# Optimization experiments

Hardware: AMD Instinct MI355X
Metric: run time of the kernel (lower is better)

The kernel has to match this reference:

```python
import jax, jax.numpy as jnp
import numpy as np

N = 50000        # nodes
E = 1_600_000    # edges (avg degree 32)
G = 512          # graphs
F_IN = 9         # node features
H = 64           # hidden dim
ED = 1           # edge feature dim


def _lin(k, fo, fi):
    w = jax.random.normal(k, (fo, fi), jnp.float32) * (1.0 / np.sqrt(fi))
    b = jnp.zeros((fo,), jnp.float32)
    return w, b


def setup_inputs() -> dict:
    key = jax.random.key(0)
    ks = jax.random.split(key, 16)
    x = jax.random.normal(ks[0], (N, F_IN), jnp.float32)
    edge_index = jax.random.randint(ks[1], (2, E), 0, N, dtype=jnp.int64)
    edge_attr = jax.random.normal(ks[2], (E, ED), jnp.float32)
    batch = jnp.sort(jax.random.randint(ks[3], (N,), 0, G, dtype=jnp.int64))
    B_total = jax.random.uniform(ks[4], (G,), jnp.float32) * 100.0
    terminal_mask = jax.random.randint(ks[5], (N,), 0, 2, dtype=jnp.int32)
    c_cost = jax.random.uniform(ks[6], (N,), jnp.float32)
    # conv1: edge lin (ED->F_IN), nn = Linear(F_IN,H), Linear(H,H)
    e1_w, e1_b = _lin(ks[7], F_IN, ED)
    w1a, b1a = _lin(ks[8], H, F_IN)
    w1b, b1b = _lin(ks[9], H, H)
    # conv2: edge lin (ED->H), nn = Linear(H,H), Linear(H,H)
    e2_w, e2_b = _lin(ks[10], H, ED)
    w2a, b2a = _lin(ks[11], H, H)
    w2b, b2b = _lin(ks[12], H, H)
    # readout: Linear(H,H//2), Linear(H//2,1)
    wr1, br1 = _lin(ks[13], H // 2, H)
    wr2, br2 = _lin(ks[14], 1, H // 2)
    return dict(x=x, edge_index=edge_index, edge_attr=edge_attr, batch=batch,
                B_total=B_total, terminal_mask=terminal_mask, c_cost=c_cost,
                e1_w=e1_w, e1_b=e1_b, w1a=w1a, b1a=b1a, w1b=w1b, b1b=b1b,
                e2_w=e2_w, e2_b=e2_b, w2a=w2a, b2a=b2a, w2b=w2b, b2b=b2b,
                wr1=wr1, br1=br1, wr2=wr2, br2=br2)


def _gine(x, src, dst, edge_attr, ew, eb, wa, ba, wb, bb):
    # GINEConv (eps=0): nn(x + sum_j relu(x_j + W_e e_ji))
    e = edge_attr @ ew.T + eb                    # [E, F]
    m = jax.nn.relu(x[src] + e)                  # [E, F] gather + edge fuse
    aggr = jax.ops.segment_sum(m, dst, num_segments=N)  # scatter-add -> [N, F]
    h = x + aggr
    h = jax.nn.relu(h @ wa.T + ba)
    h = jax.nn.relu(h @ wb.T + bb)
    return h


def reference(x, edge_index, edge_attr, batch, B_total, terminal_mask, c_cost,
              e1_w, e1_b, w1a, b1a, w1b, b1b,
              e2_w, e2_b, w2a, b2a, w2b, b2b,
              wr1, br1, wr2, br2):
    src, dst = edge_index[0], edge_index[1]
    h = _gine(x, src, dst, edge_attr, e1_w, e1_b, w1a, b1a, w1b, b1b)
    h = _gine(h, src, dst, edge_attr, e2_w, e2_b, w2a, b2a, w2b, b2b)
    pi_raw = jax.nn.sigmoid((jax.nn.relu(h @ wr1.T + br1) @ wr2.T + br2))[:, 0]
    pi_raw = pi_raw * (1.0 - terminal_mask.astype(jnp.float32))
    node_expenses = pi_raw * c_cost
    total_expenses = jax.ops.segment_sum(node_expenses, batch, num_segments=G)
    ratio = jnp.minimum(B_total[batch] / (total_expenses[batch] + 1e-12), 1.0)
    return pi_raw * ratio
```

## Files before the change

kernel.cpp:

```cpp
#include <hip/hip_runtime.h>
#include <hip/hip_fp16.h>
#include <math.h>

#define N_NODES 50000
#define N_EDGES 1600000
#define N_GRAPHS 512
#define F_IN 9
#define H 64
#define N_BUCKETS ((N_NODES + 255) >> 8)
#define EPB 4096
#define N_SBLK ((N_EDGES + EPB - 1) / EPB)
#define FINE_CAP 10240

typedef _Float16 f16x8 __attribute__((ext_vector_type(8)));
typedef float f32x4 __attribute__((ext_vector_type(4)));

__device__ __forceinline__ void pack_weights_body(
        const float* __restrict__ w1a, const float* __restrict__ w1b,
        const float* __restrict__ w2a, const float* __restrict__ w2b,
        const float* __restrict__ wr1,
        __half* __restrict__ pk1Ah, __half* __restrict__ pk1Al,
        __half* __restrict__ pk1Bh, __half* __restrict__ pk1Bl,
        __half* __restrict__ pkAh, __half* __restrict__ pkAl,
        __half* __restrict__ pkBh, __half* __restrict__ pkBl,
        __half* __restrict__ pkRh, __half* __restrict__ pkRl) {
    int t = threadIdx.x;
    for (int i = t; i < 2048; i += 512) {
        int j = i & 7, l = (i >> 3) & 63, tt = i >> 9;
        int q = l >> 4, n = l & 15;
        int k = q * 8 + j;
        float v = (k < F_IN) ? w1a[(tt * 16 + n) * F_IN + k] : 0.f;
        __half h = __float2half(v);
        pk1Ah[i] = h; pk1Al[i] = __float2half(v - __half2float(h));
    }
    for (int i = t; i < 4096; i += 512) {
        int j = i & 7, l = (i >> 3) & 63, c = (i >> 9) & 1, tt = i >> 10;
        int q = l >> 4, n = l & 15;
        int src = (tt * 16 + n) * H + c * 32 + q * 8 + j;
        float v1 = w1b[src], wa = w2a[src], wb = w2b[src];
        __half h1 = __float2half(v1), ah = __float2half(wa), bh = __float2half(wb);
        pk1Bh[i] = h1; pk1Bl[i] = __float2half(v1 - __half2float(h1));
        pkAh[i] = ah; pkAl[i] = __float2half(wa - __half2float(ah));
        pkBh[i] = bh; pkBl[i] = __float2half(wb - __half2float(bh));
    }
    for (int i = t; i < 2048; i += 512) {
        int j = i & 7, l = (i >> 3) & 63, c = (i >> 9) & 1, tt = i >> 10;
        int q = l >> 4, n = l & 15;
        float wr = wr1[(tt * 16 + n) * H + c * 32 + q * 8 + j];
        __half rh = __float2half(wr);
        pkRh[i] = rh; pkRl[i] = __float2half(wr - __half2float(rh));
    }
}

__global__ void __launch_bounds__(512)
bucket_scatter(const int* __restrict__ ei,
               const float* __restrict__ ea,
               int* __restrict__ bnext,
               uint2* __restrict__ ebuk,
               const float* __restrict__ w1a,
               const float* __restrict__ w1b,
               const float* __restrict__ w2a,
               const float* __restrict__ w2b,
               const float* __restrict__ wr1,
               __half* pk1Ah, __half* pk1Al,
               __half* pk1Bh, __half* pk1Bl,
               __half* pkAh, __half* pkAl,
               __half* pkBh, __half* pkBl,
               __half* pkRh, __half* pkRl) {
    if (blockIdx.x == 0) {
        pack_weights_body(w1a, w1b, w2a, w2b, wr1, pk1Ah, pk1Al, pk1Bh, pk1Bl,
                          pkAh, pkAl, pkBh, pkBl, pkRh, pkRl);
        return;
    }
    __shared__ int cnt[N_BUCKETS];
    __shared__ int gbase[N_BUCKETS];
    for (int i = threadIdx.x; i < N_BUCKETS; i += 512) cnt[i] = 0;
    __syncthreads();
    int base = (blockIdx.x - 1) * EPB;
    int rk[8];
    unsigned pay[8];
#pragma unroll
    for (int j = 0; j < 8; ++j) {
        int e = base + j * 512 + threadIdx.x;
        rk[j] = -1;
        if (e < N_EDGES) {
            int d = ei[N_EDGES + e];
            int s = ei[e];
            float a = ea[e];
            pay[j] = ((unsigned)s << 16) |
                     (unsigned)__half_as_ushort(__float2half(a));
            int b = d >> 8;
            int r = atomicAdd(&cnt[b], 1);
            rk[j] = (b << 21) | ((d & 255) << 13) | r;
        }
    }
    __syncthreads();
    for (int i = threadIdx.x; i < N_BUCKETS; i += 512)
        gbase[i] = cnt[i] ? atomicAdd(&bnext[i], cnt[i]) : 0;
    __syncthreads();
#pragma unroll
    for (int j = 0; j < 8; ++j) {
        if (rk[j] < 0) continue;
        int b = rk[j] >> 21, dl = (rk[j] >> 13) & 255, r = rk[j] & 8191;
        int slot = gbase[b] + r;
        if (slot >= FINE_CAP) continue;
        ebuk[(size_t)b * FINE_CAP + slot] = make_uint2(pay[j], (unsigned)dl);
    }
}

__global__ void __launch_bounds__(512)
bucket_fine(const uint2* __restrict__ ebuk,
            const int* __restrict__ bnext,
            unsigned* __restrict__ ep4,
            int* __restrict__ starts, int* __restrict__ deg) {
    __shared__ unsigned sorted[FINE_CAP];
    __shared__ int cntN[256], offN[256], nxtN[256];
    __shared__ int wsum[4];
    int b = blockIdx.x;
    int base = b * FINE_CAP;
    int count = bnext[b];
    if (count > FINE_CAP) count = FINE_CAP;
    int tid = threadIdx.x;
    if (tid < 256) cntN[tid] = 0;
    __syncthreads();
    uint2 ev[20];
#pragma unroll
    for (int k = 0; k < 20; ++k) {
        int i = tid + k * 512;
        ev[k] = (i < count) ? ebuk[base + i] : make_uint2(0u, 0xFFFFFFFFu);
    }
#pragma unroll
    for (int k = 0; k < 20; ++k)
        if (ev[k].y < 256u) atomicAdd(&cntN[ev[k].y], 1);
    __syncthreads();
    int lane = tid & 63, wid = tid >> 6;
    int v = 0, incl = 0;
    if (tid < 256) {
        v = cntN[tid]; incl = v;
#pragma unroll
        for (int off = 1; off < 64; off <<= 1) {
            int t = __shfl_up(incl, off, 64);
            if (lane >= off) incl += t;
        }
        if (lane == 63) wsum[wid] = incl;
    }
    __syncthreads();
    if (tid < 256) {
        int woff = 0;
        for (int w = 0; w < wid; ++w) woff += wsum[w];
        int excl = woff + incl - v;
        offN[tid] = excl;
        nxtN[tid] = 0;
        int n = (b << 8) + tid;
        if (n < N_NODES) { starts[n] = base + excl; deg[n] = v; }
    }
    __syncthreads();
#pragma unroll
    for (int k = 0; k < 20; ++k) {
        if (ev[k].y < 256u) {
            int r = atomicAdd(&nxtN[ev[k].y], 1);
            sorted[offN[ev[k].y] + r] = ev[k].x;
        }
    }
    __syncthreads();
    for (int i = tid; i < count; i += 512)
        ep4[base + i] = sorted[i];
}

#define UNPACK_ATTR(P) __half2float(__ushort_as_half((unsigned short)((P) & 0xffffu)))

__global__ void agg1_kernel(const float* __restrict__ x,
                            const int* __restrict__ starts,
                            const int* __restrict__ deg,
                            const unsigned* __restrict__ ep4,
                            const float* __restrict__ e1w,
                            const float* __restrict__ e1b,
                            float* __restrict__ xs) {
    int n = blockIdx.x * (blockDim.x >> 6) + (threadIdx.x >> 6);
    int lane = threadIdx.x & 63;
    if (n >= N_NODES) return;
    int slot = lane >> 4;
    int f = lane & 15;
    int s0 = starts[n], dg = deg[n];
    bool act = f < F_IN;
    float wf = act ? e1w[f] : 0.f;
    float bf = act ? e1b[f] : 0.f;
    float acc = 0.f;
    int j = slot;
    for (; j + 12 < dg; j += 16) {
        unsigned pa = ep4[s0 + j];
        unsigned pb = ep4[s0 + j + 4];
        unsigned pc = ep4[s0 + j + 8];
        unsigned pd = ep4[s0 + j + 12];
        float xa_ = act ? x[(pa >> 16) * F_IN + f] : 0.f;
        float xb_ = act ? x[(pb >> 16) * F_IN + f] : 0.f;
        float xc_ = act ? x[(pc >> 16) * F_IN + f] : 0.f;
        float xd_ = act ? x[(pd >> 16) * F_IN + f] : 0.f;
        if (act) {
            acc += fmaxf(xa_ + UNPACK_ATTR(pa) * wf + bf, 0.f)
                 + fmaxf(xb_ + UNPACK_ATTR(pb) * wf + bf, 0.f)
                 + fmaxf(xc_ + UNPACK_ATTR(pc) * wf + bf, 0.f)
                 + fmaxf(xd_ + UNPACK_ATTR(pd) * wf + bf, 0.f);
        }
    }
    for (; j < dg; j += 4) {
        unsigned p = ep4[s0 + j];
        float xv = act ? x[(p >> 16) * F_IN + f] : 0.f;
        float m = xv + UNPACK_ATTR(p) * wf + bf;
        acc += act ? fmaxf(m, 0.f) : 0.f;
    }
    acc += __shfl_xor(acc, 16, 64);
    acc += __shfl_xor(acc, 32, 64);
    if (lane < 32)
        xs[n * 32 + lane] = (lane < F_IN) ? x[n * F_IN + lane] + acc : 0.f;
}

__device__ __forceinline__ void split8(const float* __restrict__ v,
                                       f16x8& hi, f16x8& lo) {
#pragma unroll
    for (int j = 0; j < 8; ++j) {
        _Float16 h = (_Float16)v[j];
        hi[j] = h;
        lo[j] = (_Float16)(v[j] - (float)h);
    }
}

#define TILE3(C, A0H, A0L, A1H, A1L, PH, PL, T) do {                          \
        f16x8 b0h = *(const f16x8*)((PH) + (((T) * 2 + 0) * 64 + lane) * 8);  \
        f16x8 b0l = *(const f16x8*)((PL) + (((T) * 2 + 0) * 64 + lane) * 8);  \
        f16x8 b1h = *(const f16x8*)((PH) + (((T) * 2 + 1) * 64 + lane) * 8);  \
        f16x8 b1l = *(const f16x8*)((PL) + (((T) * 2 + 1) * 64 + lane) * 8);  \
        C = __builtin_amdgcn_mfma_f32_16x16x32_f16(A0H, b0h, C, 0, 0, 0);     \
        C = __builtin_amdgcn_mfma_f32_16x16x32_f16(A0L, b0h, C, 0, 0, 0);     \
        C = __builtin_amdgcn_mfma_f32_16x16x32_f16(A0H, b0l, C, 0, 0, 0);     \
        C = __builtin_amdgcn_mfma_f32_16x16x32_f16(A1H, b1h, C, 0, 0, 0);     \
        C = __builtin_amdgcn_mfma_f32_16x16x32_f16(A1L, b1h, C, 0, 0, 0);     \
        C = __builtin_amdgcn_mfma_f32_16x16x32_f16(A1H, b1l, C, 0, 0, 0);     \
    } while (0)

__global__ void node1_kernel(const float* __restrict__ xs,
                             const __half* __restrict__ pk1Ah, const __half* __restrict__ pk1Al,
                             const float* __restrict__ b1a,
                             const __half* __restrict__ pk1Bh, const __half* __restrict__ pk1Bl,
                             const float* __restrict__ b1b,
                             __half* __restrict__ h1) {
    __shared__ float hbuf[4][16][68];
    int wv = threadIdx.x >> 6;
    int lane = threadIdx.x & 63;
    int gwave = blockIdx.x * 4 + wv;
    bool active = gwave < (N_NODES / 16);
    int base = active ? gwave * 16 : 0;
    int m = lane & 15, q = lane >> 4;
    const _Float16* pAh = (const _Float16*)pk1Ah;
    const _Float16* pAl = (const _Float16*)pk1Al;
    const _Float16* pBh = (const _Float16*)pk1Bh;
    const _Float16* pBl = (const _Float16*)pk1Bl;

    f16x8 ah, al;
    split8(xs + (size_t)(base + m) * 32 + q * 8, ah, al);
#pragma unroll
    for (int t = 0; t < 4; ++t) {
        f32x4 c = {0.f, 0.f, 0.f, 0.f};
        f16x8 bh = *(const f16x8*)(pAh + (t * 64 + lane) * 8);
        f16x8 bl = *(const f16x8*)(pAl + (t * 64 + lane) * 8);
        c = __builtin_amdgcn_mfma_f32_16x16x32_f16(ah, bh, c, 0, 0, 0);
        c = __builtin_amdgcn_mfma_f32_16x16x32_f16(al, bh, c, 0, 0, 0);
        c = __builtin_amdgcn_mfma_f32_16x16x32_f16(ah, bl, c, 0, 0, 0);
        float bias = b1a[t * 16 + m];
#pragma unroll
        for (int r = 0; r < 4; ++r)
            hbuf[wv][q * 4 + r][t * 16 + m] = fmaxf(c[r] + bias, 0.f);
    }
    __syncthreads();
    f16x8 a0h, a0l, a1h, a1l;
    split8(&hbuf[wv][m][q * 8], a0h, a0l);
    split8(&hbuf[wv][m][32 + q * 8], a1h, a1l);
    float tmp[4][4];
#pragma unroll
    for (int t = 0; t < 4; ++t) {
        f32x4 c = {0.f, 0.f, 0.f, 0.f};
        TILE3(c, a0h, a0l, a1h, a1l, pBh, pBl, t);
        float bias = b1b[t * 16 + m];
#pragma unroll
        for (int r = 0; r < 4; ++r)
            tmp[t][r] = fmaxf(c[r] + bias, 0.f);
    }
    __syncthreads();
#pragma unroll
    for (int t = 0; t < 4; ++t)
#pragma unroll
        for (int r = 0; r < 4; ++r)
            hbuf[wv][q * 4 + r][t * 16 + m] = tmp[t][r];
    __syncthreads();
    if (active) {
        int nn = lane >> 2, part = lane & 3;
        f16x8 vlo, vhi;
        const float* rlo = &hbuf[wv][nn][part * 8];
        const float* rhi = &hbuf[wv][nn][32 + part * 8];
#pragma unroll
        for (int j = 0; j < 8; ++j) {
            vlo[j] = (_Float16)rlo[j];
            vhi[j] = (_Float16)rhi[j];
        }
        *(f16x8*)(h1 + (size_t)(base + nn) * 64 + part * 8) = vlo;
        *(f16x8*)(h1 + (size_t)(base + nn) * 64 + 32 + part * 8) = vhi;
    }
}

__global__ void aggphase2_kernel(const __half* __restrict__ h1,
                                 const int* __restrict__ starts,
                                 const int* __restrict__ deg,
                                 const unsigned* __restrict__ ep4,
                                 const float* __restrict__ ew,
                                 const float* __restrict__ eb,
                                 float* __restrict__ htot) {
    int xcd = blockIdx.x & 7;
    int hoff = (xcd >> 2) * 32;
    int grp = (blockIdx.x >> 3) * 4 + (xcd & 3);
    int wv = threadIdx.x >> 6;
    int n = grp * 4 + wv;
    int lane = threadIdx.x & 63;
    if (n >= N_NODES) return;
    int par = lane >> 5;
    int fh = lane & 31;
    int f = hoff + fh;
    int s0 = starts[n], dg = deg[n];
    const unsigned* ep = ep4 + s0;
    float wf = ew[f], bf = eb[f];
    float acc = 0.f;
#define EDGE1(P, V) acc += fmaxf((V) + UNPACK_ATTR(P) * wf + bf, 0.f)
    int j = 0;
    for (; j + 16 <= dg; j += 16) {
        unsigned p0 = ep[j +  0 + par], p1 = ep[j +  2 + par];
        unsigned p2 = ep[j +  4 + par], p3 = ep[j +  6 + par];
        unsigned p4 = ep[j +  8 + par], p5 = ep[j + 10 + par];
        unsigned p6 = ep[j + 12 + par], p7 = ep[j + 14 + par];
        float v0 = __half2float(h1[(size_t)(p0 >> 16) * 64 + f]);
        float v1 = __half2float(h1[(size_t)(p1 >> 16) * 64 + f]);
        float v2 = __half2float(h1[(size_t)(p2 >> 16) * 64 + f]);
        float v3 = __half2float(h1[(size_t)(p3 >> 16) * 64 + f]);
        float v4 = __half2float(h1[(size_t)(p4 >> 16) * 64 + f]);
        float v5 = __half2float(h1[(size_t)(p5 >> 16) * 64 + f]);
        float v6 = __half2float(h1[(size_t)(p6 >> 16) * 64 + f]);
        float v7 = __half2float(h1[(size_t)(p7 >> 16) * 64 + f]);
        EDGE1(p0, v0); EDGE1(p1, v1); EDGE1(p2, v2); EDGE1(p3, v3);
        EDGE1(p4, v4); EDGE1(p5, v5); EDGE1(p6, v6); EDGE1(p7, v7);
    }
    for (; j + 2 <= dg; j += 2) {
        unsigned p = ep[j + par];
        float v = __half2float(h1[(size_t)(p >> 16) * 64 + f]);
        EDGE1(p, v);
    }
    if (j < dg && par == 0) {
        unsigned p = ep[j];
        float v = __half2float(h1[(size_t)(p >> 16) * 64 + f]);
        EDGE1(p, v);
    }
#undef EDGE1
    acc += __shfl_xor(acc, 32, 64);
    if (par == 0) {
        float self = __half2float(h1[(size_t)n * 64 + f]);
        htot[(size_t)n * 64 + f] = self + acc;
    }
}

__global__ void node2_kernel(const float* __restrict__ htot,
                             const __half* __restrict__ pkAh, const __half* __restrict__ pkAl,
                             const float* __restrict__ b2a,
                             const __half* __restrict__ pkBh, const __half* __restrict__ pkBl,
                             const float* __restrict__ b2b,
                             const __half* __restrict__ pkRh, const __half* __restrict__ pkRl,
                             const float* __restrict__ br1,
                             const float* __restrict__ wr2,
                             const float* __restrict__ br2,
                             const int* __restrict__ term,
                             const int* __restrict__ batch,
                             const float* __restrict__ ccost,
                             float* __restrict__ pi,
                             float* __restrict__ te) {
    __shared__ float hbuf[4][16][68];
    int wv = threadIdx.x >> 6;
    int lane = threadIdx.x & 63;
    int gwave = blockIdx.x * 4 + wv;
    bool active = gwave < (N_NODES / 16);
    int base = active ? gwave * 16 : 0;
    int m = lane & 15, q = lane >> 4;
    const _Float16* pAh = (const _Float16*)pkAh;
    const _Float16* pAl = (const _Float16*)pkAl;
    const _Float16* pBh = (const _Float16*)pkBh;
    const _Float16* pBl = (const _Float16*)pkBl;
    const _Float16* pRh = (const _Float16*)pkRh;
    const _Float16* pRl = (const _Float16*)pkRl;

    f16x8 a0h, a0l, a1h, a1l;
    {
        const float* hrow = htot + (size_t)(base + m) * 64;
        split8(hrow + q * 8, a0h, a0l);
        split8(hrow + 32 + q * 8, a1h, a1l);
    }
#pragma unroll
    for (int t = 0; t < 4; ++t) {
        f32x4 c = {0.f, 0.f, 0.f, 0.f};
        TILE3(c, a0h, a0l, a1h, a1l, pAh, pAl, t);
        float bias = b2a[t * 16 + m];
#pragma unroll
        for (int r = 0; r < 4; ++r)
            hbuf[wv][q * 4 + r][t * 16 + m] = fmaxf(c[r] + bias, 0.f);
    }
    __syncthreads();
    split8(&hbuf[wv][m][q * 8], a0h, a0l);
    split8(&hbuf[wv][m][32 + q * 8], a1h, a1l);
    float tmp[4][4];
#pragma unroll
    for (int t = 0; t < 4; ++t) {
        f32x4 c = {0.f, 0.f, 0.f, 0.f};
        TILE3(c, a0h, a0l, a1h, a1l, pBh, pBl, t);
        float bias = b2b[t * 16 + m];
#pragma unroll
        for (int r = 0; r < 4; ++r)
            tmp[t][r] = fmaxf(c[r] + bias, 0.f);
    }
    __syncthreads();
#pragma unroll
    for (int t = 0; t < 4; ++t)
#pragma unroll
        for (int r = 0; r < 4; ++r)
            hbuf[wv][q * 4 + r][t * 16 + m] = tmp[t][r];
    __syncthreads();
    split8(&hbuf[wv][m][q * 8], a0h, a0l);
    split8(&hbuf[wv][m][32 + q * 8], a1h, a1l);
    float partial[4] = {0.f, 0.f, 0.f, 0.f};
#pragma unroll
    for (int t = 0; t < 2; ++t) {
        f32x4 c = {0.f, 0.f, 0.f, 0.f};
        TILE3(c, a0h, a0l, a1h, a1l, pRh, pRl, t);
        float bias = br1[t * 16 + m];
        float wv2 = wr2[t * 16 + m];
#pragma unroll
        for (int r = 0; r < 4; ++r)
            partial[r] += fmaxf(c[r] + bias, 0.f) * wv2;
    }
#pragma unroll
    for (int off = 1; off < 16; off <<= 1) {
        partial[0] += __shfl_xor(partial[0], off, 64);
        partial[1] += __shfl_xor(partial[1], off, 64);
        partial[2] += __shfl_xor(partial[2], off, 64);
        partial[3] += __shfl_xor(partial[3], off, 64);
    }
    if (active && m == 0) {
#pragma unroll
        for (int r = 0; r < 4; ++r) {
            int n = base + q * 4 + r;
            float z = partial[r] + br2[0];
            float sig = 1.f / (1.f + expf(-z));
            float pv = sig * (1.f - (float)term[n]);
            pi[n] = pv;
            float contrib = pv * ccost[n];
            if (contrib != 0.f) atomicAdd(&te[batch[n]], contrib);
        }
    }
}

__global__ void final_kernel(const float* __restrict__ pi,
                             const int* __restrict__ batch,
                             const float* __restrict__ Btot,
                             const float* __restrict__ te,
                             float* __restrict__ out) {
    int n = blockIdx.x * blockDim.x + threadIdx.x;
    if (n >= N_NODES) return;
    int b = batch[n];
    float ratio = fminf(Btot[b] / (te[b] + 1e-12f), 1.f);
    out[n] = pi[n] * ratio;
}

extern "C" void kernel_launch(void* const* d_in, const int* in_sizes, int n_in,
                              void* d_out, int out_size, void* d_ws, size_t ws_size,
                              hipStream_t stream) {
    const float* x     = (const float*)d_in[0];
    const int*   ei    = (const int*)d_in[1];
    const float* ea    = (const float*)d_in[2];
    const int*   batch = (const int*)d_in[3];
    const float* Btot  = (const float*)d_in[4];
    const int*   term  = (const int*)d_in[5];
    const float* ccost = (const float*)d_in[6];
    const float* e1w   = (const float*)d_in[7];
    const float* e1b   = (const float*)d_in[8];
    const float* w1a   = (const float*)d_in[9];
    const float* b1a   = (const float*)d_in[10];
    const float* w1b   = (const float*)d_in[11];
    const float* b1b   = (const float*)d_in[12];
    const float* e2w   = (const float*)d_in[13];
    const float* e2b   = (const float*)d_in[14];
    const float* w2a   = (const float*)d_in[15];
    const float* b2a   = (const float*)d_in[16];
    const float* w2b   = (const float*)d_in[17];
    const float* b2b   = (const float*)d_in[18];
    const float* wr1   = (const float*)d_in[19];
    const float* br1   = (const float*)d_in[20];
    const float* wr2   = (const float*)d_in[21];
    const float* br2   = (const float*)d_in[22];

    char* p = (char*)d_ws;
    int*      bnext  = (int*)p;      p += sizeof(int)      * 256;
    float*    te     = (float*)p;    p += sizeof(float)    * N_GRAPHS;
    int*      starts = (int*)p;      p += sizeof(int)      * N_NODES;
    int*      deg    = (int*)p;      p += sizeof(int)      * N_NODES;
    p = (char*)(((size_t)p + 15) & ~(size_t)15);
    uint2*    ebuk   = (uint2*)p;    p += sizeof(uint2)    * (size_t)N_BUCKETS * FINE_CAP;
    unsigned* ep4    = (unsigned*)p; p += sizeof(unsigned) * (size_t)N_BUCKETS * FINE_CAP;
    __half*   h1     = (__half*)p;   p += sizeof(__half)   * (size_t)N_NODES * 64;
    float*    htot   = (float*)p;    p += sizeof(float)    * (size_t)N_NODES * 64;
    float*    xs     = (float*)p;    p += sizeof(float)    * (size_t)N_NODES * 32;
    float*    pi     = (float*)p;    p += sizeof(float)    * N_NODES;
    __half*   pk1Ah  = (__half*)p;   p += sizeof(__half)   * 2048;
    __half*   pk1Al  = (__half*)p;   p += sizeof(__half)   * 2048;
    __half*   pk1Bh  = (__half*)p;   p += sizeof(__half)   * 4096;
    __half*   pk1Bl  = (__half*)p;   p += sizeof(__half)   * 4096;
    __half*   pkAh   = (__half*)p;   p += sizeof(__half)   * 4096;
    __half*   pkAl   = (__half*)p;   p += sizeof(__half)   * 4096;
    __half*   pkBh   = (__half*)p;   p += sizeof(__half)   * 4096;
    __half*   pkBl   = (__half*)p;   p += sizeof(__half)   * 4096;
    __half*   pkRh   = (__half*)p;   p += sizeof(__half)   * 2048;
    __half*   pkRl   = (__half*)p;   p += sizeof(__half)   * 2048;
    float*    out    = (float*)d_out;

    hipMemsetAsync(d_ws, 0, sizeof(int) * 256 + sizeof(float) * N_GRAPHS, stream);

    bucket_scatter<<<1 + N_SBLK, 512, 0, stream>>>(ei, ea, bnext, ebuk,
                                                   w1a, w1b, w2a, w2b, wr1,
                                                   pk1Ah, pk1Al, pk1Bh, pk1Bl,
                                                   pkAh, pkAl, pkBh, pkBl, pkRh, pkRl);
    bucket_fine<<<N_BUCKETS, 512, 0, stream>>>(ebuk, bnext, ep4, starts, deg);
    agg1_kernel<<<(N_NODES + 3) / 4, 256, 0, stream>>>(x, starts, deg, ep4, e1w, e1b, xs);
    node1_kernel<<<(N_NODES / 16 + 3) / 4, 256, 0, stream>>>(xs, pk1Ah, pk1Al, b1a,
                                                             pk1Bh, pk1Bl, b1b, h1);
    aggphase2_kernel<<<25000, 256, 0, stream>>>(h1, starts, deg, ep4,
                                                e2w, e2b, htot);
    node2_kernel<<<(N_NODES / 16 + 3) / 4, 256, 0, stream>>>(htot,
                                                             pkAh, pkAl, b2a,
                                                             pkBh, pkBl, b2b,
                                                             pkRh, pkRl, br1,
                                                             wr2, br2, term,
                                                             batch, ccost, pi, te);
    final_kernel<<<(N_NODES + 255) / 256, 256, 0, stream>>>(pi, batch, Btot, te, out);
}
```

Measured before the change: 265.3 us.

## Process full 64-feature rows per wave in layer-2 aggregation with half2 gathers

The layer-2 aggregation kernel no longer splits each node's 64 features across two XCD-mapped blocks. Each wave now handles a whole node, with each lane reading a half2 (two features) per gathered neighbour row, which halves the block count and the edge-list and index reads per node. The htot and xs outputs use nontemporal stores. The trade-off is that the XCD-aware split, which kept each half of h1 resident in a separate L2, is dropped, so each L2 may now see the full h1 gather footprint.

```diff
diff --git a/kernel.cpp b/kernel.cpp
--- a/kernel.cpp
+++ b/kernel.cpp
@@ -14,6 +14,7 @@
 
 typedef _Float16 f16x8 __attribute__((ext_vector_type(8)));
 typedef float f32x4 __attribute__((ext_vector_type(4)));
+typedef float f32x2 __attribute__((ext_vector_type(2)));
 
 __device__ __forceinline__ void pack_weights_body(
         const float* __restrict__ w1a, const float* __restrict__ w1b,
@@ -211,8 +212,10 @@
     }
     acc += __shfl_xor(acc, 16, 64);
     acc += __shfl_xor(acc, 32, 64);
-    if (lane < 32)
-        xs[n * 32 + lane] = (lane < F_IN) ? x[n * F_IN + lane] + acc : 0.f;
+    if (lane < 32) {
+        float v = (lane < F_IN) ? x[n * F_IN + lane] + acc : 0.f;
+        __builtin_nontemporal_store(v, xs + n * 32 + lane);
+    }
 }
 
 __device__ __forceinline__ void split8(const float* __restrict__ v,
@@ -314,53 +317,54 @@
                                  const float* __restrict__ ew,
                                  const float* __restrict__ eb,
                                  float* __restrict__ htot) {
-    int xcd = blockIdx.x & 7;
-    int hoff = (xcd >> 2) * 32;
-    int grp = (blockIdx.x >> 3) * 4 + (xcd & 3);
-    int wv = threadIdx.x >> 6;
-    int n = grp * 4 + wv;
+    int n = blockIdx.x * (blockDim.x >> 6) + (threadIdx.x >> 6);
     int lane = threadIdx.x & 63;
     if (n >= N_NODES) return;
-    int par = lane >> 5;
-    int fh = lane & 31;
-    int f = hoff + fh;
+    int half = lane >> 5;
+    int l = lane & 31;
     int s0 = starts[n], dg = deg[n];
     const unsigned* ep = ep4 + s0;
-    float wf = ew[f], bf = eb[f];
-    float acc = 0.f;
-#define EDGE1(P, V) acc += fmaxf((V) + UNPACK_ATTR(P) * wf + bf, 0.f)
+    const unsigned* h1u = (const unsigned*)h1;
+    float2 w2 = *(const float2*)(ew + 2 * l);
+    float2 b2 = *(const float2*)(eb + 2 * l);
+    float acc0 = 0.f, acc1 = 0.f;
+#define EDGE2(P, V) do {                                                   \
+        float a_ = UNPACK_ATTR(P);                                         \
+        __half2 hv_ = *(const __half2*)&(V);                               \
+        float2 vf_ = __half22float2(hv_);                                  \
+        acc0 += fmaxf(vf_.x + a_ * w2.x + b2.x, 0.f);                      \
+        acc1 += fmaxf(vf_.y + a_ * w2.y + b2.y, 0.f);                      \
+    } while (0)
     int j = 0;
-    for (; j + 16 <= dg; j += 16) {
-        unsigned p0 = ep[j +  0 + par], p1 = ep[j +  2 + par];
-        unsigned p2 = ep[j +  4 + par], p3 = ep[j +  6 + par];
-        unsigned p4 = ep[j +  8 + par], p5 = ep[j + 10 + par];
-        unsigned p6 = ep[j + 12 + par], p7 = ep[j + 14 + par];
-        float v0 = __half2float(h1[(size_t)(p0 >> 16) * 64 + f]);
-        float v1 = __half2float(h1[(size_t)(p1 >> 16) * 64 + f]);
-        float v2 = __half2float(h1[(size_t)(p2 >> 16) * 64 + f]);
-        float v3 = __half2float(h1[(size_t)(p3 >> 16) * 64 + f]);
-        float v4 = __half2float(h1[(size_t)(p4 >> 16) * 64 + f]);
-        float v5 = __half2float(h1[(size_t)(p5 >> 16) * 64 + f]);
-        float v6 = __half2float(h1[(size_t)(p6 >> 16) * 64 + f]);
-        float v7 = __half2float(h1[(size_t)(p7 >> 16) * 64 + f]);
-        EDGE1(p0, v0); EDGE1(p1, v1); EDGE1(p2, v2); EDGE1(p3, v3);
-        EDGE1(p4, v4); EDGE1(p5, v5); EDGE1(p6, v6); EDGE1(p7, v7);
+    for (; j + 8 <= dg; j += 8) {
+        unsigned p0 = ep[j + 0 + half], p1 = ep[j + 2 + half];
+        unsigned p2 = ep[j + 4 + half], p3 = ep[j + 6 + half];
+        unsigned v0 = h1u[(size_t)(p0 >> 16) * 32 + l];
+        unsigned v1 = h1u[(size_t)(p1 >> 16) * 32 + l];
+        unsigned v2 = h1u[(size_t)(p2 >> 16) * 32 + l];
+        unsigned v3 = h1u[(size_t)(p3 >> 16) * 32 + l];
+        EDGE2(p0, v0); EDGE2(p1, v1); EDGE2(p2, v2); EDGE2(p3, v3);
     }
     for (; j + 2 <= dg; j += 2) {
-        unsigned p = ep[j + par];
-        float v = __half2float(h1[(size_t)(p >> 16) * 64 + f]);
-        EDGE1(p, v);
-    }
-    if (j < dg && par == 0) {
+        unsigned p = ep[j + half];
+        unsigned v = h1u[(size_t)(p >> 16) * 32 + l];
+        EDGE2(p, v);
+    }
+    if (j < dg && half == 0) {
         unsigned p = ep[j];
-        float v = __half2float(h1[(size_t)(p >> 16) * 64 + f]);
-        EDGE1(p, v);
-    }
-#undef EDGE1
-    acc += __shfl_xor(acc, 32, 64);
-    if (par == 0) {
-        float self = __half2float(h1[(size_t)n * 64 + f]);
-        htot[(size_t)n * 64 + f] = self + acc;
+        unsigned v = h1u[(size_t)(p >> 16) * 32 + l];
+        EDGE2(p, v);
+    }
+#undef EDGE2
+    acc0 += __shfl_xor(acc0, 32, 64);
+    acc1 += __shfl_xor(acc1, 32, 64);
+    if (half == 0) {
+        unsigned sv = h1u[(size_t)n * 32 + l];
+        float2 sf = __half22float2(*(const __half2*)&sv);
+        f32x2 o;
+        o[0] = sf.x + acc0;
+        o[1] = sf.y + acc1;
+        __builtin_nontemporal_store(o, (f32x2*)(htot + (size_t)n * 64 + 2 * l));
     }
 }
 
@@ -534,8 +538,8 @@
     agg1_kernel<<<(N_NODES + 3) / 4, 256, 0, stream>>>(x, starts, deg, ep4, e1w, e1b, xs);
     node1_kernel<<<(N_NODES / 16 + 3) / 4, 256, 0, stream>>>(xs, pk1Ah, pk1Al, b1a,
                                                              pk1Bh, pk1Bl, b1b, h1);
-    aggphase2_kernel<<<25000, 256, 0, stream>>>(h1, starts, deg, ep4,
-                                                e2w, e2b, htot);
+    aggphase2_kernel<<<(N_NODES + 3) / 4, 256, 0, stream>>>(h1, starts, deg, ep4,
+                                                            e2w, e2b, htot);
     node2_kernel<<<(N_NODES / 16 + 3) / 4, 256, 0, stream>>>(htot,
                                                              pkAh, pkAl, b2a,
                                                              pkBh, pkBl, b2b,
```

New measurement: 236.2 us. 11.0% less time.
